# Performance work log

Hardware: AMD Instinct MI355X
Metric: run time of the kernel (lower is better)

## Reference

```python
import jax, jax.numpy as jnp
import numpy as np

IN_FEATURES = 4096
OUT_FEATURES = 14336
GROUP_SIZE = 128  # in_features grouped: 4096 / 128 = 32 groups
N_GROUPS = IN_FEATURES // GROUP_SIZE


def setup_inputs() -> dict:
    key = jax.random.key(0)
    k_x, k_q, k_s, k_zb, k_b = jax.random.split(key, 5)
    x = jax.random.normal(k_x, (8, 32, IN_FEATURES), dtype=jnp.float32)
    # uint8-style affine-quantized weights packed as (in_features, out_features)
    quant_kernel = jax.random.randint(k_q, (IN_FEATURES, OUT_FEATURES), 0, 256, dtype=jnp.int32)
    # per-group scales / zero-point biases: (n_groups, out_features)
    quant_scales = (jax.random.uniform(k_s, (N_GROUPS, OUT_FEATURES), dtype=jnp.float32) + 0.5) * 0.01
    quant_biases = jax.random.normal(k_zb, (N_GROUPS, OUT_FEATURES), dtype=jnp.float32) * 0.01
    bias = jax.random.normal(k_b, (OUT_FEATURES,), dtype=jnp.float32) * 0.02
    return {"x": x, "quant_kernel": quant_kernel, "quant_scales": quant_scales,
            "quant_biases": quant_biases, "bias": bias}


def reference(x, quant_kernel, quant_scales, quant_biases, bias):
    # Affine group-wise dequant: w[f, o] = q[f, o] * scale[f//G, o] + zp_bias[f//G, o]
    q = quant_kernel.astype(jnp.float32).reshape(N_GROUPS, GROUP_SIZE, OUT_FEATURES)
    w = q * quant_scales[:, None, :] + quant_biases[:, None, :]
    w = w.reshape(IN_FEATURES, OUT_FEATURES)
    # y = x @ W + b  (x: [B, S, K], W: [K, N])
    y = jnp.einsum("bsk,kn->bsn", x, w) + bias
    return y
```

## Files before the change

kernel.cpp:

```cpp
#include <hip/hip_runtime.h>
#include <hip/hip_bf16.h>

#define K_DIM 4096
#define N_DIM 14336
#define M_DIM 256
#define BN 64
#define BK 128
#define NITER 32
#define RS 136

typedef __attribute__((ext_vector_type(4))) float f32x4;
typedef __attribute__((ext_vector_type(8))) short short8;

__device__ __forceinline__ unsigned short f2bf(float f) {
    union { float f; unsigned u; } v; v.f = f;
    unsigned r = v.u + 0x7fffu + ((v.u >> 16) & 1u);
    return (unsigned short)(r >> 16);
}

__global__ void convert_x_kernel(const float* __restrict__ x,
                                 unsigned short* __restrict__ xf) {
    int t = blockIdx.x * blockDim.x + threadIdx.x;
    int chunk = t >> 6;
    int lane  = t & 63;
    int ktile = chunk >> 4;
    int mtile = chunk & 15;
    int m = mtile * 16 + (lane & 15);
    int k = ktile * 32 + ((lane >> 4) << 3);
    const float* xp = x + (size_t)m * K_DIM + k;
    float4 lo = *(const float4*)xp;
    float4 hi = *(const float4*)(xp + 4);
    union { unsigned short s[8]; int4 v; } o;
    o.s[0] = f2bf(lo.x); o.s[1] = f2bf(lo.y); o.s[2] = f2bf(lo.z); o.s[3] = f2bf(lo.w);
    o.s[4] = f2bf(hi.x); o.s[5] = f2bf(hi.y); o.s[6] = f2bf(hi.z); o.s[7] = f2bf(hi.w);
    *(int4*)(xf + ((size_t)t << 3)) = o.v;
}

template<bool USE_WS>
__global__ __launch_bounds__(512, 2)
void plq_gemm_kernel(const float* __restrict__ x,
                     const unsigned short* __restrict__ xf,
                     const int* __restrict__ q,
                     const float* __restrict__ qs,
                     const float* __restrict__ qb,
                     const float* __restrict__ bias,
                     float* __restrict__ out)
{
    __shared__ unsigned short wlds[2][BN * RS];

    const int tid  = threadIdx.x;
    const int lane = tid & 63;
    const int wv   = tid >> 6;
    const int wm   = wv >> 1;
    const int wn   = wv & 1;
    const int n0   = blockIdx.x * BN;

    const int tn = tid & 31;
    const int tk = tid >> 5;
    const int nl = tn * 2;
    const int kl = tk * 8;

    f32x4 acc[4][2] = {};

    int2   qr[8];
    float2 sv, zv;

    auto loadq = [&](int i) {
        const int* qp = q + (size_t)(i * BK + kl) * N_DIM + (n0 + nl);
        #pragma unroll
        for (int j = 0; j < 8; ++j)
            qr[j] = *(const int2*)(qp + (size_t)j * N_DIM);
        sv = *(const float2*)(qs + (size_t)i * N_DIM + (n0 + nl));
        zv = *(const float2*)(qb + (size_t)i * N_DIM + (n0 + nl));
    };

    auto deqw = [&](int b) {
        union { unsigned u[4]; int4 v; } p0, p1;
        #pragma unroll
        for (int j = 0; j < 4; ++j) {
            float a0 = (float)qr[2*j].x   * sv.x + zv.x;
            float a1 = (float)qr[2*j+1].x * sv.x + zv.x;
            float c0 = (float)qr[2*j].y   * sv.y + zv.y;
            float c1 = (float)qr[2*j+1].y * sv.y + zv.y;
            p0.u[j] = (unsigned)f2bf(a0) | ((unsigned)f2bf(a1) << 16);
            p1.u[j] = (unsigned)f2bf(c0) | ((unsigned)f2bf(c1) << 16);
        }
        *(int4*)&wlds[b][(nl + 0) * RS + kl] = p0.v;
        *(int4*)&wlds[b][(nl + 1) * RS + kl] = p1.v;
    };

    auto compute = [&](int i, int cur) {
        short8 afr[4][4];
        if (USE_WS) {
            #pragma unroll
            for (int ks = 0; ks < 4; ++ks)
                #pragma unroll
                for (int mf = 0; mf < 4; ++mf) {
                    int chunk = (i * 4 + ks) * 16 + (wm * 4 + mf);
                    afr[ks][mf] = *(const short8*)(xf + ((size_t)chunk << 9) + (size_t)(lane << 3));
                }
        } else {
            #pragma unroll
            for (int ks = 0; ks < 4; ++ks)
                #pragma unroll
                for (int mf = 0; mf < 4; ++mf) {
                    int m = wm * 64 + mf * 16 + (lane & 15);
                    int k = i * BK + ks * 32 + ((lane >> 4) << 3);
                    const float* xp = x + (size_t)m * K_DIM + k;
                    float4 lo = *(const float4*)xp;
                    float4 hi = *(const float4*)(xp + 4);
                    union { unsigned short s[8]; short8 v; } u;
                    u.s[0] = f2bf(lo.x); u.s[1] = f2bf(lo.y); u.s[2] = f2bf(lo.z); u.s[3] = f2bf(lo.w);
                    u.s[4] = f2bf(hi.x); u.s[5] = f2bf(hi.y); u.s[6] = f2bf(hi.z); u.s[7] = f2bf(hi.w);
                    afr[ks][mf] = u.v;
                }
        }
        #pragma unroll
        for (int ks = 0; ks < 4; ++ks) {
            const int kb = ks * 32 + ((lane >> 4) << 3);
            short8 b0 = *(const short8*)&wlds[cur][(wn * 32 +      (lane & 15)) * RS + kb];
            short8 b1 = *(const short8*)&wlds[cur][(wn * 32 + 16 + (lane & 15)) * RS + kb];
            #pragma unroll
            for (int mf = 0; mf < 4; ++mf) {
                acc[mf][0] = __builtin_amdgcn_mfma_f32_16x16x32_bf16(afr[ks][mf], b0, acc[mf][0], 0, 0, 0);
                acc[mf][1] = __builtin_amdgcn_mfma_f32_16x16x32_bf16(afr[ks][mf], b1, acc[mf][1], 0, 0, 0);
            }
        }
    };

    loadq(0);
    deqw(0);
    __syncthreads();

    for (int i = 0; i < NITER; ++i) {
        const int cur = i & 1;
        if (i + 1 < NITER) loadq(i + 1);
        compute(i, cur);
        if (i + 1 < NITER) deqw(cur ^ 1);
        __syncthreads();
    }

    #pragma unroll
    for (int nf = 0; nf < 2; ++nf) {
        const int n = n0 + wn * 32 + nf * 16 + (lane & 15);
        const float bb = bias[n];
        #pragma unroll
        for (int mf = 0; mf < 4; ++mf) {
            const int m0 = wm * 64 + mf * 16 + ((lane >> 4) << 2);
            #pragma unroll
            for (int r = 0; r < 4; ++r)
                out[(size_t)(m0 + r) * N_DIM + n] = acc[mf][nf][r] + bb;
        }
    }
}

extern "C" void kernel_launch(void* const* d_in, const int* in_sizes, int n_in,
                              void* d_out, int out_size, void* d_ws, size_t ws_size,
                              hipStream_t stream) {
    const float* x    = (const float*)d_in[0];
    const int*   qk   = (const int*)d_in[1];
    const float* qs   = (const float*)d_in[2];
    const float* qb   = (const float*)d_in[3];
    const float* bias = (const float*)d_in[4];
    float* out = (float*)d_out;

    const size_t xf_bytes = (size_t)M_DIM * K_DIM * sizeof(unsigned short);
    if (ws_size >= xf_bytes) {
        unsigned short* xf = (unsigned short*)d_ws;
        convert_x_kernel<<<512, 256, 0, stream>>>(x, xf);
        plq_gemm_kernel<true><<<N_DIM / BN, 512, 0, stream>>>(x, xf, qk, qs, qb, bias, out);
    } else {
        plq_gemm_kernel<false><<<N_DIM / BN, 512, 0, stream>>>(x, nullptr, qk, qs, qb, bias, out);
    }
}
```

Baseline: 93.49 us.

## Deepen weight prefetch to two stages with dual register sets and lighter barriers

The loop now alternates two register sets for the quantized weight loads, so global loads for tile i+2 are issued while tile i is computed. This gives a prefetch distance of two iterations instead of one, to hide more HBM latency. The LDS buffers are split into separate arrays and the loop is unrolled by two. __syncthreads is replaced by a custom barrier that waits only on lgkmcnt, so outstanding global loads are not drained at each barrier. Occupancy hint drops to one block per SM to make room for the extra registers, which risks losing the latency hiding that two resident blocks gave.

Result: slower. 105.7 us (+13.1%).

```diff
diff --git a/kernel.cpp b/kernel.cpp
--- a/kernel.cpp
+++ b/kernel.cpp
@@ -16,6 +16,12 @@
     union { float f; unsigned u; } v; v.f = f;
     unsigned r = v.u + 0x7fffu + ((v.u >> 16) & 1u);
     return (unsigned short)(r >> 16);
+}
+
+__device__ __forceinline__ void lds_barrier() {
+    asm volatile("s_waitcnt lgkmcnt(0)" ::: "memory");
+    __builtin_amdgcn_s_barrier();
+    asm volatile("" ::: "memory");
 }
 
 __global__ void convert_x_kernel(const float* __restrict__ x,
@@ -37,7 +43,7 @@
 }
 
 template<bool USE_WS>
-__global__ __launch_bounds__(512, 2)
+__global__ __launch_bounds__(512, 1)
 void plq_gemm_kernel(const float* __restrict__ x,
                      const unsigned short* __restrict__ xf,
                      const int* __restrict__ q,
@@ -46,7 +52,8 @@
                      const float* __restrict__ bias,
                      float* __restrict__ out)
 {
-    __shared__ unsigned short wlds[2][BN * RS];
+    __shared__ unsigned short wlds0[BN * RS];
+    __shared__ unsigned short wlds1[BN * RS];
 
     const int tid  = threadIdx.x;
     const int lane = tid & 63;
@@ -62,34 +69,56 @@
 
     f32x4 acc[4][2] = {};
 
-    int2   qr[8];
-    float2 sv, zv;
-
-    auto loadq = [&](int i) {
+    int2   qA[8], qB[8];
+    float2 svA, zvA, svB, zvB;
+
+    auto loadqA = [&](int i) {
         const int* qp = q + (size_t)(i * BK + kl) * N_DIM + (n0 + nl);
         #pragma unroll
         for (int j = 0; j < 8; ++j)
-            qr[j] = *(const int2*)(qp + (size_t)j * N_DIM);
-        sv = *(const float2*)(qs + (size_t)i * N_DIM + (n0 + nl));
-        zv = *(const float2*)(qb + (size_t)i * N_DIM + (n0 + nl));
-    };
-
-    auto deqw = [&](int b) {
+            qA[j] = *(const int2*)(qp + (size_t)j * N_DIM);
+        svA = *(const float2*)(qs + (size_t)i * N_DIM + (n0 + nl));
+        zvA = *(const float2*)(qb + (size_t)i * N_DIM + (n0 + nl));
+    };
+    auto loadqB = [&](int i) {
+        const int* qp = q + (size_t)(i * BK + kl) * N_DIM + (n0 + nl);
+        #pragma unroll
+        for (int j = 0; j < 8; ++j)
+            qB[j] = *(const int2*)(qp + (size_t)j * N_DIM);
+        svB = *(const float2*)(qs + (size_t)i * N_DIM + (n0 + nl));
+        zvB = *(const float2*)(qb + (size_t)i * N_DIM + (n0 + nl));
+    };
+
+    auto deqA = [&](unsigned short* dst) {
         union { unsigned u[4]; int4 v; } p0, p1;
         #pragma unroll
         for (int j = 0; j < 4; ++j) {
-            float a0 = (float)qr[2*j].x   * sv.x + zv.x;
-            float a1 = (float)qr[2*j+1].x * sv.x + zv.x;
-            float c0 = (float)qr[2*j].y   * sv.y + zv.y;
-            float c1 = (float)qr[2*j+1].y * sv.y + zv.y;
+            float a0 = (float)qA[2*j].x   * svA.x + zvA.x;
+            float a1 = (float)qA[2*j+1].x * svA.x + zvA.x;
+            float c0 = (float)qA[2*j].y   * svA.y + zvA.y;
+            float c1 = (float)qA[2*j+1].y * svA.y + zvA.y;
             p0.u[j] = (unsigned)f2bf(a0) | ((unsigned)f2bf(a1) << 16);
             p1.u[j] = (unsigned)f2bf(c0) | ((unsigned)f2bf(c1) << 16);
         }
-        *(int4*)&wlds[b][(nl + 0) * RS + kl] = p0.v;
-        *(int4*)&wlds[b][(nl + 1) * RS + kl] = p1.v;
-    };
-
-    auto compute = [&](int i, int cur) {
+        *(int4*)&dst[(nl + 0) * RS + kl] = p0.v;
+        *(int4*)&dst[(nl + 1) * RS + kl] = p1.v;
+    };
+    auto deqB = [&](unsigned short* dst) {
+        union { unsigned u[4]; int4 v; } p0, p1;
+        #pragma unroll
+        for (int j = 0; j < 4; ++j) {
+            float a0 = (float)qB[2*j].x   * svB.x + zvB.x;
+            float a1 = (float)qB[2*j+1].x * svB.x + zvB.x;
+            float c0 = (float)qB[2*j].y   * svB.y + zvB.y;
+            float c1 = (float)qB[2*j+1].y * svB.y + zvB.y;
+            p0.u[j] = (unsigned)f2bf(a0) | ((unsigned)f2bf(a1) << 16);
+            p1.u[j] = (unsigned)f2bf(c0) | ((unsigned)f2bf(c1) << 16);
+        }
+        *(int4*)&dst[(nl + 0) * RS + kl] = p0.v;
+        *(int4*)&dst[(nl + 1) * RS + kl] = p1.v;
+    };
+
+    auto compute = [&](int i, const unsigned short* buf) {
         short8 afr[4][4];
         if (USE_WS) {
             #pragma unroll
@@ -118,8 +147,8 @@
         #pragma unroll
         for (int ks = 0; ks < 4; ++ks) {
             const int kb = ks * 32 + ((lane >> 4) << 3);
-            short8 b0 = *(const short8*)&wlds[cur][(wn * 32 +      (lane & 15)) * RS + kb];
-            short8 b1 = *(const short8*)&wlds[cur][(wn * 32 + 16 + (lane & 15)) * RS + kb];
+            short8 b0 = *(const short8*)&buf[(wn * 32 +      (lane & 15)) * RS + kb];
+            short8 b1 = *(const short8*)&buf[(wn * 32 + 16 + (lane & 15)) * RS + kb];
             #pragma unroll
             for (int mf = 0; mf < 4; ++mf) {
                 acc[mf][0] = __builtin_amdgcn_mfma_f32_16x16x32_bf16(afr[ks][mf], b0, acc[mf][0], 0, 0, 0);
@@ -128,16 +157,25 @@
         }
     };
 
-    loadq(0);
-    deqw(0);
-    __syncthreads();
-
-    for (int i = 0; i < NITER; ++i) {
-        const int cur = i & 1;
-        if (i + 1 < NITER) loadq(i + 1);
-        compute(i, cur);
-        if (i + 1 < NITER) deqw(cur ^ 1);
-        __syncthreads();
+    loadqA(0);
+    loadqB(1);
+    deqA(wlds0);
+    lds_barrier();
+
+    #pragma unroll 1
+    for (int ii = 0; ii < NITER / 2; ++ii) {
+        const int i = 2 * ii;
+        if (i + 2 < NITER) loadqA(i + 2);
+        compute(i, wlds0);
+        deqB(wlds1);
+        lds_barrier();
+
+        if (i + 3 < NITER) loadqB(i + 3);
+        compute(i + 1, wlds1);
+        if (i + 2 < NITER) {
+            deqA(wlds0);
+            lds_barrier();
+        }
     }
 
     #pragma unroll
```

## Rewrite workspace GEMM path with async global-to-LDS loads and deeper pipeline

Applied to the files above, without the earlier changes.

Adds a new main kernel that stages bf16 activations and raw int32 quantized weights into shared memory with global_load_lds DMA, keeping a three-deep ring buffer for the weights. Scales and zero points are preloaded into LDS once per block. Tiles are smaller (BN 32, BK 64), giving twice as many blocks at one block per CU. The goal is to overlap the dominant 235 MB weight stream with dequant and MFMA work, at the cost of more LDS traffic, manual waitcnt synchronisation, and lower MFMA work per barrier.

After: 157.5 us. 68.5% more time.

```diff
diff --git a/kernel.cpp b/kernel.cpp
--- a/kernel.cpp
+++ b/kernel.cpp
@@ -4,10 +4,10 @@
 #define K_DIM 4096
 #define N_DIM 14336
 #define M_DIM 256
-#define BN 64
-#define BK 128
-#define NITER 32
-#define RS 136
+#define BN 32
+#define BK 64
+#define NITER 64
+#define RS 80
 
 typedef __attribute__((ext_vector_type(4))) float f32x4;
 typedef __attribute__((ext_vector_type(8))) short short8;
@@ -16,6 +16,12 @@
     union { float f; unsigned u; } v; v.f = f;
     unsigned r = v.u + 0x7fffu + ((v.u >> 16) & 1u);
     return (unsigned short)(r >> 16);
+}
+
+__device__ __forceinline__ void glds16(const void* g, void* l) {
+    __builtin_amdgcn_global_load_lds(
+        (const __attribute__((address_space(1))) void*)g,
+        (__attribute__((address_space(3))) void*)l, 16, 0, 0);
 }
 
 __global__ void convert_x_kernel(const float* __restrict__ x,
@@ -36,44 +42,156 @@
     *(int4*)(xf + ((size_t)t << 3)) = o.v;
 }
 
-template<bool USE_WS>
+__global__ __launch_bounds__(512, 1)
+void plq_gemm_v3(const unsigned short* __restrict__ xf,
+                 const int* __restrict__ q,
+                 const float* __restrict__ qs,
+                 const float* __restrict__ qb,
+                 const float* __restrict__ bias,
+                 float* __restrict__ out)
+{
+    __shared__ unsigned short Ab[2][16384];
+    __shared__ int            rq[3][2048];
+    __shared__ unsigned short wb[2][BN * RS];
+    __shared__ float          scb[32 * BN];
+    __shared__ float          zbb[32 * BN];
+
+    const int tid  = threadIdx.x;
+    const int lane = tid & 63;
+    const int wv   = tid >> 6;
+    const int n0   = blockIdx.x * BN;
+
+    const int dq_n  = tid & 31;
+    const int dq_k0 = (tid >> 5) * 4;
+
+    auto issueA = [&](int t, int p) {
+        const char* src = (const char*)xf + (size_t)t * 32768 + wv * 4096 + (lane << 4);
+        char* dst = (char*)&Ab[p][0] + wv * 4096;
+        glds16(src,        dst);
+        glds16(src + 1024, dst + 1024);
+        glds16(src + 2048, dst + 2048);
+        glds16(src + 3072, dst + 3072);
+    };
+    auto issueQ = [&](int t) {
+        const int* src = q + (size_t)(t * BK + wv * 8 + (lane >> 3)) * N_DIM
+                           + n0 + ((lane & 7) << 2);
+        char* dst = (char*)&rq[t % 3][0] + wv * 1024;
+        glds16(src, dst);
+    };
+    auto dequant = [&](int t, unsigned short* dstw) {
+        const int* rp = &rq[t % 3][0];
+        const int g = t >> 1;
+        float s = scb[g * BN + dq_n];
+        float z = zbb[g * BN + dq_n];
+        int v0 = rp[(dq_k0 + 0) * 32 + dq_n];
+        int v1 = rp[(dq_k0 + 1) * 32 + dq_n];
+        int v2 = rp[(dq_k0 + 2) * 32 + dq_n];
+        int v3 = rp[(dq_k0 + 3) * 32 + dq_n];
+        float f0 = (float)v0 * s + z;
+        float f1 = (float)v1 * s + z;
+        float f2 = (float)v2 * s + z;
+        float f3 = (float)v3 * s + z;
+        union { unsigned u[2]; double d; } pk;
+        pk.u[0] = (unsigned)f2bf(f0) | ((unsigned)f2bf(f1) << 16);
+        pk.u[1] = (unsigned)f2bf(f2) | ((unsigned)f2bf(f3) << 16);
+        *(double*)&dstw[dq_n * RS + dq_k0] = pk.d;
+    };
+
+    f32x4 acc[2][2] = {};
+    auto compute = [&](int p) {
+        const unsigned short* ab = &Ab[p][0];
+        const unsigned short* bb = &wb[p][0];
+        #pragma unroll
+        for (int ks = 0; ks < 2; ++ks) {
+            const int kb = ks * 32 + ((lane >> 4) << 3);
+            short8 b0 = *(const short8*)&bb[(     (lane & 15)) * RS + kb];
+            short8 b1 = *(const short8*)&bb[(16 + (lane & 15)) * RS + kb];
+            short8 a0 = *(const short8*)&ab[(ks * 16 + 2 * wv + 0) * 512 + (lane << 3)];
+            short8 a1 = *(const short8*)&ab[(ks * 16 + 2 * wv + 1) * 512 + (lane << 3)];
+            acc[0][0] = __builtin_amdgcn_mfma_f32_16x16x32_bf16(a0, b0, acc[0][0], 0, 0, 0);
+            acc[0][1] = __builtin_amdgcn_mfma_f32_16x16x32_bf16(a0, b1, acc[0][1], 0, 0, 0);
+            acc[1][0] = __builtin_amdgcn_mfma_f32_16x16x32_bf16(a1, b0, acc[1][0], 0, 0, 0);
+            acc[1][1] = __builtin_amdgcn_mfma_f32_16x16x32_bf16(a1, b1, acc[1][1], 0, 0, 0);
+        }
+    };
+
+    {
+        int g = tid >> 4;
+        int c = (tid & 15) * 2;
+        float2 s2 = *(const float2*)(qs + (size_t)g * N_DIM + n0 + c);
+        float2 z2 = *(const float2*)(qb + (size_t)g * N_DIM + n0 + c);
+        *(float2*)&scb[g * BN + c] = s2;
+        *(float2*)&zbb[g * BN + c] = z2;
+    }
+    issueA(0, 0);
+    issueQ(0); issueQ(1); issueQ(2);
+    asm volatile("s_waitcnt vmcnt(1)" ::: "memory");
+    asm volatile("s_waitcnt lgkmcnt(0)" ::: "memory");
+    __builtin_amdgcn_s_barrier();
+    dequant(0, &wb[0][0]);
+    asm volatile("s_waitcnt lgkmcnt(0)" ::: "memory");
+    __builtin_amdgcn_s_barrier();
+
+    #pragma unroll 1
+    for (int i = 0; i < NITER; ++i) {
+        const int p = i & 1;
+        if (i + 1 < NITER) issueA(i + 1, p ^ 1);
+        if (i + 3 < NITER) issueQ(i + 3);
+        compute(p);
+        if (i + 1 < NITER) dequant(i + 1, &wb[p ^ 1][0]);
+        if (i + 3 < NITER) asm volatile("s_waitcnt vmcnt(1)" ::: "memory");
+        else               asm volatile("s_waitcnt vmcnt(0)" ::: "memory");
+        asm volatile("s_waitcnt lgkmcnt(0)" ::: "memory");
+        __builtin_amdgcn_s_barrier();
+    }
+
+    #pragma unroll
+    for (int nf = 0; nf < 2; ++nf) {
+        const int n = n0 + nf * 16 + (lane & 15);
+        const float bb2 = bias[n];
+        #pragma unroll
+        for (int mf = 0; mf < 2; ++mf) {
+            const int m0 = wv * 32 + mf * 16 + ((lane >> 4) << 2);
+            #pragma unroll
+            for (int r = 0; r < 4; ++r)
+                out[(size_t)(m0 + r) * N_DIM + n] = acc[mf][nf][r] + bb2;
+        }
+    }
+}
+
+#define FBN 64
+#define FBK 128
+#define FNITER 32
+#define FRS 136
 __global__ __launch_bounds__(512, 2)
-void plq_gemm_kernel(const float* __restrict__ x,
-                     const unsigned short* __restrict__ xf,
-                     const int* __restrict__ q,
-                     const float* __restrict__ qs,
-                     const float* __restrict__ qb,
-                     const float* __restrict__ bias,
-                     float* __restrict__ out)
+void plq_gemm_fb(const float* __restrict__ x,
+                 const int* __restrict__ q,
+                 const float* __restrict__ qs,
+                 const float* __restrict__ qb,
+                 const float* __restrict__ bias,
+                 float* __restrict__ out)
 {
-    __shared__ unsigned short wlds[2][BN * RS];
-
+    __shared__ unsigned short wlds[2][FBN * FRS];
     const int tid  = threadIdx.x;
     const int lane = tid & 63;
     const int wv   = tid >> 6;
     const int wm   = wv >> 1;
     const int wn   = wv & 1;
-    const int n0   = blockIdx.x * BN;
-
-    const int tn = tid & 31;
-    const int tk = tid >> 5;
-    const int nl = tn * 2;
-    const int kl = tk * 8;
+    const int n0   = blockIdx.x * FBN;
+    const int nl = (tid & 31) * 2;
+    const int kl = (tid >> 5) * 8;
 
     f32x4 acc[4][2] = {};
-
     int2   qr[8];
     float2 sv, zv;
 
     auto loadq = [&](int i) {
-        const int* qp = q + (size_t)(i * BK + kl) * N_DIM + (n0 + nl);
-        #pragma unroll
-        for (int j = 0; j < 8; ++j)
-            qr[j] = *(const int2*)(qp + (size_t)j * N_DIM);
+        const int* qp = q + (size_t)(i * FBK + kl) * N_DIM + (n0 + nl);
+        #pragma unroll
+        for (int j = 0; j < 8; ++j) qr[j] = *(const int2*)(qp + (size_t)j * N_DIM);
         sv = *(const float2*)(qs + (size_t)i * N_DIM + (n0 + nl));
         zv = *(const float2*)(qb + (size_t)i * N_DIM + (n0 + nl));
     };
-
     auto deqw = [&](int b) {
         union { unsigned u[4]; int4 v; } p0, p1;
         #pragma unroll
@@ -85,41 +203,30 @@
             p0.u[j] = (unsigned)f2bf(a0) | ((unsigned)f2bf(a1) << 16);
             p1.u[j] = (unsigned)f2bf(c0) | ((unsigned)f2bf(c1) << 16);
         }
-        *(int4*)&wlds[b][(nl + 0) * RS + kl] = p0.v;
-        *(int4*)&wlds[b][(nl + 1) * RS + kl] = p1.v;
-    };
-
+        *(int4*)&wlds[b][(nl + 0) * FRS + kl] = p0.v;
+        *(int4*)&wlds[b][(nl + 1) * FRS + kl] = p1.v;
+    };
     auto compute = [&](int i, int cur) {
         short8 afr[4][4];
-        if (USE_WS) {
-            #pragma unroll
-            for (int ks = 0; ks < 4; ++ks)
-                #pragma unroll
-                for (int mf = 0; mf < 4; ++mf) {
-                    int chunk = (i * 4 + ks) * 16 + (wm * 4 + mf);
-                    afr[ks][mf] = *(const short8*)(xf + ((size_t)chunk << 9) + (size_t)(lane << 3));
-                }
-        } else {
-            #pragma unroll
-            for (int ks = 0; ks < 4; ++ks)
-                #pragma unroll
-                for (int mf = 0; mf < 4; ++mf) {
-                    int m = wm * 64 + mf * 16 + (lane & 15);
-                    int k = i * BK + ks * 32 + ((lane >> 4) << 3);
-                    const float* xp = x + (size_t)m * K_DIM + k;
-                    float4 lo = *(const float4*)xp;
-                    float4 hi = *(const float4*)(xp + 4);
-                    union { unsigned short s[8]; short8 v; } u;
-                    u.s[0] = f2bf(lo.x); u.s[1] = f2bf(lo.y); u.s[2] = f2bf(lo.z); u.s[3] = f2bf(lo.w);
-                    u.s[4] = f2bf(hi.x); u.s[5] = f2bf(hi.y); u.s[6] = f2bf(hi.z); u.s[7] = f2bf(hi.w);
-                    afr[ks][mf] = u.v;
-                }
-        }
+        #pragma unroll
+        for (int ks = 0; ks < 4; ++ks)
+            #pragma unroll
+            for (int mf = 0; mf < 4; ++mf) {
+                int m = wm * 64 + mf * 16 + (lane & 15);
+                int k = i * FBK + ks * 32 + ((lane >> 4) << 3);
+                const float* xp = x + (size_t)m * K_DIM + k;
+                float4 lo = *(const float4*)xp;
+                float4 hi = *(const float4*)(xp + 4);
+                union { unsigned short s[8]; short8 v; } u;
+                u.s[0] = f2bf(lo.x); u.s[1] = f2bf(lo.y); u.s[2] = f2bf(lo.z); u.s[3] = f2bf(lo.w);
+                u.s[4] = f2bf(hi.x); u.s[5] = f2bf(hi.y); u.s[6] = f2bf(hi.z); u.s[7] = f2bf(hi.w);
+                afr[ks][mf] = u.v;
+            }
         #pragma unroll
         for (int ks = 0; ks < 4; ++ks) {
             const int kb = ks * 32 + ((lane >> 4) << 3);
-            short8 b0 = *(const short8*)&wlds[cur][(wn * 32 +      (lane & 15)) * RS + kb];
-            short8 b1 = *(const short8*)&wlds[cur][(wn * 32 + 16 + (lane & 15)) * RS + kb];
+            short8 b0 = *(const short8*)&wlds[cur][(wn * 32 +      (lane & 15)) * FRS + kb];
+            short8 b1 = *(const short8*)&wlds[cur][(wn * 32 + 16 + (lane & 15)) * FRS + kb];
             #pragma unroll
             for (int mf = 0; mf < 4; ++mf) {
                 acc[mf][0] = __builtin_amdgcn_mfma_f32_16x16x32_bf16(afr[ks][mf], b0, acc[mf][0], 0, 0, 0);
@@ -128,18 +235,14 @@
         }
     };
 
-    loadq(0);
-    deqw(0);
-    __syncthreads();
-
-    for (int i = 0; i < NITER; ++i) {
+    loadq(0); deqw(0); __syncthreads();
+    for (int i = 0; i < FNITER; ++i) {
         const int cur = i & 1;
-        if (i + 1 < NITER) loadq(i + 1);
+        if (i + 1 < FNITER) loadq(i + 1);
         compute(i, cur);
-        if (i + 1 < NITER) deqw(cur ^ 1);
+        if (i + 1 < FNITER) deqw(cur ^ 1);
         __syncthreads();
     }
-
     #pragma unroll
     for (int nf = 0; nf < 2; ++nf) {
         const int n = n0 + wn * 32 + nf * 16 + (lane & 15);
@@ -168,8 +271,8 @@
     if (ws_size >= xf_bytes) {
         unsigned short* xf = (unsigned short*)d_ws;
         convert_x_kernel<<<512, 256, 0, stream>>>(x, xf);
-        plq_gemm_kernel<true><<<N_DIM / BN, 512, 0, stream>>>(x, xf, qk, qs, qb, bias, out);
+        plq_gemm_v3<<<N_DIM / BN, 512, 0, stream>>>(xf, qk, qs, qb, bias, out);
     } else {
-        plq_gemm_kernel<false><<<N_DIM / BN, 512, 0, stream>>>(x, nullptr, qk, qs, qb, bias, out);
-    }
-}
+        plq_gemm_fb<<<N_DIM / FBN, 512, 0, stream>>>(x, qk, qs, qb, bias, out);
+    }
+}
```

## Split M into halves with smaller N/K tiles and swizzled block mapping

Applied to the files above, without the earlier changes.

The GEMM kernel is retiled from 64-wide N tiles over all 256 rows to 32-wide N tiles over 128-row halves with BK=64. This quadruples the grid to 896 blocks of 256 threads, and each wave now handles a 32x32 output tile. Block IDs are swizzled across groups of 8, and double buffering uses two named LDS buffers with a 2x-unrolled loop. The intent is higher occupancy and more parallelism. The cost is that each quantized weight column is now loaded and dequantized twice, once per M half, which doubles weight traffic and dequant work.

After: 111.9 us. +19.7%, slower.

```diff
diff --git a/kernel.cpp b/kernel.cpp
--- a/kernel.cpp
+++ b/kernel.cpp
@@ -4,10 +4,11 @@
 #define K_DIM 4096
 #define N_DIM 14336
 #define M_DIM 256
-#define BN 64
-#define BK 128
-#define NITER 32
-#define RS 136
+#define BM 128
+#define BN 32
+#define BK 64
+#define NITER 64
+#define RS 72
 
 typedef __attribute__((ext_vector_type(4))) float f32x4;
 typedef __attribute__((ext_vector_type(8))) short short8;
@@ -37,119 +38,137 @@
 }
 
 template<bool USE_WS>
-__global__ __launch_bounds__(512, 2)
-void plq_gemm_kernel(const float* __restrict__ x,
-                     const unsigned short* __restrict__ xf,
-                     const int* __restrict__ q,
-                     const float* __restrict__ qs,
-                     const float* __restrict__ qb,
-                     const float* __restrict__ bias,
-                     float* __restrict__ out)
+__global__ __launch_bounds__(256, 4)
+void plq_gemm_v4(const float* __restrict__ x,
+                 const unsigned short* __restrict__ xf,
+                 const int* __restrict__ q,
+                 const float* __restrict__ qs,
+                 const float* __restrict__ qb,
+                 const float* __restrict__ bias,
+                 float* __restrict__ out)
 {
-    __shared__ unsigned short wlds[2][BN * RS];
+    __shared__ unsigned short wb0[BN * RS];
+    __shared__ unsigned short wb1[BN * RS];
 
     const int tid  = threadIdx.x;
     const int lane = tid & 63;
     const int wv   = tid >> 6;
-    const int wm   = wv >> 1;
-    const int wn   = wv & 1;
-    const int n0   = blockIdx.x * BN;
 
-    const int tn = tid & 31;
-    const int tk = tid >> 5;
-    const int nl = tn * 2;
-    const int kl = tk * 8;
+    const int bid   = blockIdx.x;
+    const int gid   = (bid & 7) * 112 + (bid >> 3);
+    const int mhalf = gid & 1;
+    const int n0    = (gid >> 1) * BN;
+    const int m0b   = mhalf * BM;
 
-    f32x4 acc[4][2] = {};
+    const int dq_n  = tid & 31;
+    const int dq_k0 = (tid >> 5) << 3;
+    const size_t qcol = (size_t)n0 + dq_n;
 
-    int2   qr[8];
-    float2 sv, zv;
+    f32x4 acc[2][2] = {};
 
-    auto loadq = [&](int i) {
-        const int* qp = q + (size_t)(i * BK + kl) * N_DIM + (n0 + nl);
+    int   qA[8], qB[8];
+    float sA, zA, sB, zB;
+
+    auto loadA = [&](int t) {
+        const int* qp = q + (size_t)(t * BK + dq_k0) * N_DIM + qcol;
         #pragma unroll
-        for (int j = 0; j < 8; ++j)
-            qr[j] = *(const int2*)(qp + (size_t)j * N_DIM);
-        sv = *(const float2*)(qs + (size_t)i * N_DIM + (n0 + nl));
-        zv = *(const float2*)(qb + (size_t)i * N_DIM + (n0 + nl));
+        for (int j = 0; j < 8; ++j) qA[j] = qp[(size_t)j * N_DIM];
+        sA = qs[(size_t)(t >> 1) * N_DIM + qcol];
+        zA = qb[(size_t)(t >> 1) * N_DIM + qcol];
+    };
+    auto loadB = [&](int t) {
+        const int* qp = q + (size_t)(t * BK + dq_k0) * N_DIM + qcol;
+        #pragma unroll
+        for (int j = 0; j < 8; ++j) qB[j] = qp[(size_t)j * N_DIM];
+        sB = qs[(size_t)(t >> 1) * N_DIM + qcol];
+        zB = qb[(size_t)(t >> 1) * N_DIM + qcol];
     };
 
-    auto deqw = [&](int b) {
-        union { unsigned u[4]; int4 v; } p0, p1;
+    auto deqA = [&]() {
+        union { unsigned u[4]; int4 v; } pk;
         #pragma unroll
         for (int j = 0; j < 4; ++j) {
-            float a0 = (float)qr[2*j].x   * sv.x + zv.x;
-            float a1 = (float)qr[2*j+1].x * sv.x + zv.x;
-            float c0 = (float)qr[2*j].y   * sv.y + zv.y;
-            float c1 = (float)qr[2*j+1].y * sv.y + zv.y;
-            p0.u[j] = (unsigned)f2bf(a0) | ((unsigned)f2bf(a1) << 16);
-            p1.u[j] = (unsigned)f2bf(c0) | ((unsigned)f2bf(c1) << 16);
+            float f0 = (float)qA[2*j]   * sA + zA;
+            float f1 = (float)qA[2*j+1] * sA + zA;
+            pk.u[j] = (unsigned)f2bf(f0) | ((unsigned)f2bf(f1) << 16);
         }
-        *(int4*)&wlds[b][(nl + 0) * RS + kl] = p0.v;
-        *(int4*)&wlds[b][(nl + 1) * RS + kl] = p1.v;
+        *(int4*)&wb0[dq_n * RS + dq_k0] = pk.v;
+    };
+    auto deqB = [&]() {
+        union { unsigned u[4]; int4 v; } pk;
+        #pragma unroll
+        for (int j = 0; j < 4; ++j) {
+            float f0 = (float)qB[2*j]   * sB + zB;
+            float f1 = (float)qB[2*j+1] * sB + zB;
+            pk.u[j] = (unsigned)f2bf(f0) | ((unsigned)f2bf(f1) << 16);
+        }
+        *(int4*)&wb1[dq_n * RS + dq_k0] = pk.v;
     };
 
-    auto compute = [&](int i, int cur) {
-        short8 afr[4][4];
-        if (USE_WS) {
-            #pragma unroll
-            for (int ks = 0; ks < 4; ++ks)
-                #pragma unroll
-                for (int mf = 0; mf < 4; ++mf) {
-                    int chunk = (i * 4 + ks) * 16 + (wm * 4 + mf);
-                    afr[ks][mf] = *(const short8*)(xf + ((size_t)chunk << 9) + (size_t)(lane << 3));
-                }
-        } else {
-            #pragma unroll
-            for (int ks = 0; ks < 4; ++ks)
-                #pragma unroll
-                for (int mf = 0; mf < 4; ++mf) {
-                    int m = wm * 64 + mf * 16 + (lane & 15);
-                    int k = i * BK + ks * 32 + ((lane >> 4) << 3);
-                    const float* xp = x + (size_t)m * K_DIM + k;
-                    float4 lo = *(const float4*)xp;
-                    float4 hi = *(const float4*)(xp + 4);
-                    union { unsigned short s[8]; short8 v; } u;
-                    u.s[0] = f2bf(lo.x); u.s[1] = f2bf(lo.y); u.s[2] = f2bf(lo.z); u.s[3] = f2bf(lo.w);
-                    u.s[4] = f2bf(hi.x); u.s[5] = f2bf(hi.y); u.s[6] = f2bf(hi.z); u.s[7] = f2bf(hi.w);
-                    afr[ks][mf] = u.v;
-                }
-        }
+    auto compute = [&](int i, const unsigned short* bb) {
+        const int mt0 = (mhalf << 3) + (wv << 1);
         #pragma unroll
-        for (int ks = 0; ks < 4; ++ks) {
+        for (int ks = 0; ks < 2; ++ks) {
+            const int kt = i * 2 + ks;
+            short8 a0, a1;
+            if (USE_WS) {
+                const unsigned short* ap = xf + ((size_t)(kt * 16 + mt0) << 9) + (lane << 3);
+                a0 = *(const short8*)ap;
+                a1 = *(const short8*)(ap + 512);
+            } else {
+                const int m = m0b + wv * 32 + (lane & 15);
+                const int k = kt * 32 + ((lane >> 4) << 3);
+                const float* xp0 = x + (size_t)m * K_DIM + k;
+                const float* xp1 = xp0 + (size_t)16 * K_DIM;
+                float4 l0 = *(const float4*)xp0, h0 = *(const float4*)(xp0 + 4);
+                float4 l1 = *(const float4*)xp1, h1 = *(const float4*)(xp1 + 4);
+                union { unsigned short s[8]; short8 v; } u0, u1;
+                u0.s[0] = f2bf(l0.x); u0.s[1] = f2bf(l0.y); u0.s[2] = f2bf(l0.z); u0.s[3] = f2bf(l0.w);
+                u0.s[4] = f2bf(h0.x); u0.s[5] = f2bf(h0.y); u0.s[6] = f2bf(h0.z); u0.s[7] = f2bf(h0.w);
+                u1.s[0] = f2bf(l1.x); u1.s[1] = f2bf(l1.y); u1.s[2] = f2bf(l1.z); u1.s[3] = f2bf(l1.w);
+                u1.s[4] = f2bf(h1.x); u1.s[5] = f2bf(h1.y); u1.s[6] = f2bf(h1.z); u1.s[7] = f2bf(h1.w);
+                a0 = u0.v; a1 = u1.v;
+            }
             const int kb = ks * 32 + ((lane >> 4) << 3);
-            short8 b0 = *(const short8*)&wlds[cur][(wn * 32 +      (lane & 15)) * RS + kb];
-            short8 b1 = *(const short8*)&wlds[cur][(wn * 32 + 16 + (lane & 15)) * RS + kb];
-            #pragma unroll
-            for (int mf = 0; mf < 4; ++mf) {
-                acc[mf][0] = __builtin_amdgcn_mfma_f32_16x16x32_bf16(afr[ks][mf], b0, acc[mf][0], 0, 0, 0);
-                acc[mf][1] = __builtin_amdgcn_mfma_f32_16x16x32_bf16(afr[ks][mf], b1, acc[mf][1], 0, 0, 0);
-            }
+            short8 b0 = *(const short8*)&bb[(     (lane & 15)) * RS + kb];
+            short8 b1 = *(const short8*)&bb[(16 + (lane & 15)) * RS + kb];
+            acc[0][0] = __builtin_amdgcn_mfma_f32_16x16x32_bf16(a0, b0, acc[0][0], 0, 0, 0);
+            acc[0][1] = __builtin_amdgcn_mfma_f32_16x16x32_bf16(a0, b1, acc[0][1], 0, 0, 0);
+            acc[1][0] = __builtin_amdgcn_mfma_f32_16x16x32_bf16(a1, b0, acc[1][0], 0, 0, 0);
+            acc[1][1] = __builtin_amdgcn_mfma_f32_16x16x32_bf16(a1, b1, acc[1][1], 0, 0, 0);
         }
     };
 
-    loadq(0);
-    deqw(0);
+    loadA(0);
+    loadB(1);
+    deqA();
     __syncthreads();
 
-    for (int i = 0; i < NITER; ++i) {
-        const int cur = i & 1;
-        if (i + 1 < NITER) loadq(i + 1);
-        compute(i, cur);
-        if (i + 1 < NITER) deqw(cur ^ 1);
+    #pragma unroll 1
+    for (int ii = 0; ii < NITER / 2; ++ii) {
+        const int i = 2 * ii;
+
+        if (i + 2 < NITER) loadA(i + 2);
+        compute(i, wb0);
+        deqB();
+        __syncthreads();
+
+        if (i + 3 < NITER) loadB(i + 3);
+        compute(i + 1, wb1);
+        if (i + 2 < NITER) deqA();
         __syncthreads();
     }
 
     #pragma unroll
     for (int nf = 0; nf < 2; ++nf) {
-        const int n = n0 + wn * 32 + nf * 16 + (lane & 15);
-        const float bb = bias[n];
+        const int n = n0 + nf * 16 + (lane & 15);
+        const float bv = bias[n];
         #pragma unroll
-        for (int mf = 0; mf < 4; ++mf) {
-            const int m0 = wm * 64 + mf * 16 + ((lane >> 4) << 2);
+        for (int mf = 0; mf < 2; ++mf) {
+            const int m0 = m0b + wv * 32 + mf * 16 + ((lane >> 4) << 2);
             #pragma unroll
             for (int r = 0; r < 4; ++r)
-                out[(size_t)(m0 + r) * N_DIM + n] = acc[mf][nf][r] + bb;
+                out[(size_t)(m0 + r) * N_DIM + n] = acc[mf][nf][r] + bv;
         }
     }
 }
@@ -164,12 +183,13 @@
     const float* bias = (const float*)d_in[4];
     float* out = (float*)d_out;
 
+    const int grid = (M_DIM / BM) * (N_DIM / BN);
     const size_t xf_bytes = (size_t)M_DIM * K_DIM * sizeof(unsigned short);
     if (ws_size >= xf_bytes) {
         unsigned short* xf = (unsigned short*)d_ws;
         convert_x_kernel<<<512, 256, 0, stream>>>(x, xf);
-        plq_gemm_kernel<true><<<N_DIM / BN, 512, 0, stream>>>(x, xf, qk, qs, qb, bias, out);
+        plq_gemm_v4<true><<<grid, 256, 0, stream>>>(x, xf, qk, qs, qb, bias, out);
     } else {
-        plq_gemm_kernel<false><<<N_DIM / BN, 512, 0, stream>>>(x, nullptr, qk, qs, qb, bias, out);
+        plq_gemm_v4<false><<<grid, 256, 0, stream>>>(x, nullptr, qk, qs, qb, bias, out);
     }
 }
```
